# Performance work log

Measured on AMD Instinct MI355X. Metric: run time of the kernel, lower is better.

## Reference

```python
import jax, jax.numpy as jnp
import numpy as np

N, Wt, Tt, DIM = 16, 256, 2048, 256
EPS = 1e-5

def silu(x):
    return x * jax.nn.sigmoid(x)

def setup_inputs() -> dict:
    key = jax.random.key(0)
    ks = jax.random.split(key, 12)
    d = {}
    d['T'] = jnp.arange(Tt, dtype=jnp.float32)
    d['durations'] = jax.random.uniform(ks[0], (N, Wt, 1), jnp.float32)
    d['features'] = jax.random.normal(ks[1], (N, Wt, DIM), jnp.float32)
    d['conv1_w'] = jax.random.normal(ks[2], (8, DIM, 3), jnp.float32) * 0.05
    d['conv1_b'] = jnp.zeros((8,), jnp.float32)
    d['bn1_g'] = jnp.ones((8,), jnp.float32)
    d['bn1_b'] = jnp.zeros((8,), jnp.float32)
    d['bn1_m'] = jnp.zeros((8,), jnp.float32)
    d['bn1_v'] = jnp.ones((8,), jnp.float32)
    d['conv2_w'] = jax.random.normal(ks[3], (8, DIM, 3), jnp.float32) * 0.05
    d['conv2_b'] = jnp.zeros((8,), jnp.float32)
    d['bn2_g'] = jnp.ones((8,), jnp.float32)
    d['bn2_b'] = jnp.zeros((8,), jnp.float32)
    d['bn2_m'] = jnp.zeros((8,), jnp.float32)
    d['bn2_v'] = jnp.ones((8,), jnp.float32)
    d['sb1_w1'] = jax.random.normal(ks[4], (10, 2), jnp.float32) * 0.3
    d['sb1_b1'] = jnp.zeros((2,), jnp.float32)
    d['sb1_w2'] = jax.random.normal(ks[5], (2, 2), jnp.float32) * 0.3
    d['sb1_b2'] = jnp.zeros((2,), jnp.float32)
    d['sb2_w1'] = jax.random.normal(ks[6], (10, 16), jnp.float32) * 0.3
    d['sb2_b1'] = jnp.zeros((16,), jnp.float32)
    d['sb2_w2'] = jax.random.normal(ks[7], (16, 16), jnp.float32) * 0.3
    d['sb2_b2'] = jnp.zeros((16,), jnp.float32)
    d['proj1_w'] = jax.random.normal(ks[8], (2, DIM), jnp.float32) * 0.3
    d['proj1_b'] = jnp.zeros((DIM,), jnp.float32)
    d['proj2_w'] = jax.random.normal(ks[9], (16, 1), jnp.float32) * 0.3
    d['proj2_b'] = jnp.zeros((1,), jnp.float32)
    return d

def _conv_bn_silu(x_ncw, w, b, g, beta, m, v):
    # Conv1d(dim->8, k=3, pad=1) + BatchNorm(eval) + SiLU
    y = jax.lax.conv_general_dilated(x_ncw, w, (1,), [(1, 1)],
                                     dimension_numbers=('NCH', 'OIH', 'NCH'))
    y = y + b[None, :, None]
    y = (y - m[None, :, None]) * jax.lax.rsqrt(v[None, :, None] + EPS)
    y = y * g[None, :, None] + beta[None, :, None]
    return silu(y)

def _swish_block(x, w1, b1, w2, b2):
    x = silu(x @ w1 + b1)
    return silu(x @ w2 + b2)

def reference(T, durations, features, conv1_w, conv1_b, bn1_g, bn1_b, bn1_m, bn1_v,
              conv2_w, conv2_b, bn2_g, bn2_b, bn2_m, bn2_v,
              sb1_w1, sb1_b1, sb1_w2, sb1_b2, sb2_w1, sb2_b1, sb2_w2, sb2_b2,
              proj1_w, proj1_b, proj2_w, proj2_b):
    feat = jnp.swapaxes(features, 1, 2)  # (N, C, W)
    n, _, w = feat.shape
    t = T.shape[0]
    left = jnp.swapaxes(_conv_bn_silu(feat, conv1_w, conv1_b, bn1_g, bn1_b, bn1_m, bn1_v), 1, 2)   # (N, W, 8)
    right = jnp.swapaxes(_conv_bn_silu(feat, conv2_w, conv2_b, bn2_g, bn2_b, bn2_m, bn2_v), 1, 2)  # (N, W, 8)
    token_end = jnp.cumsum(durations, axis=1)        # (N, W, 1)
    token_start = token_end - durations              # (N, W, 1)
    S = T[None, None, :] - token_start               # (N, W, T)
    E = token_end - T[None, None, :]                 # (N, W, T)
    left_b = jnp.broadcast_to(left[:, :, None, :], (n, w, t, 8))
    right_b = jnp.broadcast_to(right[:, :, None, :], (n, w, t, 8))
    xleft = jnp.concatenate([S[..., None], E[..., None], left_b], axis=-1)    # (N, W, T, 10)
    xright = jnp.concatenate([S[..., None], E[..., None], right_b], axis=-1)  # (N, W, T, 10)
    C = _swish_block(xleft, sb1_w1, sb1_b1, sb1_w2, sb1_b2)                   # (N, W, T, 2)
    xr = _swish_block(xright, sb2_w1, sb2_b1, sb2_w2, sb2_b2)                 # (N, W, T, 16)
    score = (xr @ proj2_w + proj2_b)[..., 0]                                  # (N, W, T)
    Wsm = jax.nn.softmax(score, axis=1)  # softmax over tokens W
    out_r = jnp.einsum('nkt,ndk->ntd', Wsm, feat)                             # (N, T, dim)
    out_l = jnp.einsum('nkt,nktp->ntp', Wsm, C) @ proj1_w + proj1_b           # (N, T, dim)
    return out_l + out_r
```

## Files before the change

kernel.cpp:

```cpp
#include <hip/hip_runtime.h>
#include <hip/hip_bf16.h>

#define NN  16
#define WT  256
#define TT  2048
#define DIM 256
#define TBT 8

typedef __attribute__((ext_vector_type(8))) short short8_t;
typedef __attribute__((ext_vector_type(4))) float f32x4;

__device__ __forceinline__ float fast_rcp(float x){ return __builtin_amdgcn_rcpf(x); }

__device__ __forceinline__ float silu_f(float x){
    return x * fast_rcp(1.0f + __expf(-x));
}

__device__ __forceinline__ unsigned short f2bf(float x){
    union { float f; unsigned u; } v; v.f = x;
    unsigned r = v.u + 0x7FFFu + ((v.u >> 16) & 1u);
    return (unsigned short)(r >> 16);
}

__device__ __forceinline__ void fma4(float4& a, float s, const float4& f){
    a.x = fmaf(s, f.x, a.x); a.y = fmaf(s, f.y, a.y);
    a.z = fmaf(s, f.z, a.z); a.w = fmaf(s, f.w, a.w);
}

__global__ __launch_bounds__(256) void prep_k(
    const float* __restrict__ dur, const float* __restrict__ feat,
    const float* __restrict__ c1w, const float* __restrict__ c1b,
    const float* __restrict__ g1,  const float* __restrict__ be1,
    const float* __restrict__ m1,  const float* __restrict__ vv1,
    const float* __restrict__ c2w, const float* __restrict__ c2b,
    const float* __restrict__ g2,  const float* __restrict__ be2,
    const float* __restrict__ m2,  const float* __restrict__ vv2,
    const float* __restrict__ sb1w1, const float* __restrict__ sb1b1,
    const float* __restrict__ sb2w1, const float* __restrict__ sb2b1,
    float* __restrict__ v1o, float* __restrict__ v2o)
{
    int w = blockIdx.x, n = blockIdx.y;
    int tid = threadIdx.x;

    __shared__ float sdur[WT];
    sdur[tid] = dur[n*WT + tid];
    __syncthreads();
    for (int off = 1; off < WT; off <<= 1){
        float v = (tid >= off) ? sdur[tid-off] : 0.0f;
        __syncthreads();
        sdur[tid] += v;
        __syncthreads();
    }
    float end   = sdur[w];
    float start = end - dur[n*WT + w];

    const float* fb = feat + (size_t)(n*WT)*DIM;
    float fm = (w > 0)    ? fb[(size_t)(w-1)*DIM + tid] : 0.0f;
    float f0 =              fb[(size_t) w   *DIM + tid];
    float fp = (w < WT-1) ? fb[(size_t)(w+1)*DIM + tid] : 0.0f;

    float pl[8], pr[8];
    #pragma unroll
    for (int o = 0; o < 8; o++){
        const float* wp = c1w + (size_t)(o*DIM + tid)*3;
        pl[o] = fmaf(fm, wp[0], fmaf(f0, wp[1], fp*wp[2]));
        const float* wq = c2w + (size_t)(o*DIM + tid)*3;
        pr[o] = fmaf(fm, wq[0], fmaf(f0, wq[1], fp*wq[2]));
    }
    #pragma unroll
    for (int o = 0; o < 8; o++){
        #pragma unroll
        for (int off = 32; off; off >>= 1){
            pl[o] += __shfl_xor(pl[o], off);
            pr[o] += __shfl_xor(pr[o], off);
        }
    }
    __shared__ float sws[4][16];
    int wave = tid >> 6, lane = tid & 63;
    if (lane == 0){
        #pragma unroll
        for (int o = 0; o < 8; o++){ sws[wave][o] = pl[o]; sws[wave][8+o] = pr[o]; }
    }
    __syncthreads();
    __shared__ float slr[16];
    if (tid < 16){
        float s = sws[0][tid] + sws[1][tid] + sws[2][tid] + sws[3][tid];
        int o = tid & 7; bool isr = tid >= 8;
        float bias = isr ? c2b[o] : c1b[o];
        float mm   = isr ? m2[o]  : m1[o];
        float vv   = isr ? vv2[o] : vv1[o];
        float gg   = isr ? g2[o]  : g1[o];
        float bb   = isr ? be2[o] : be1[o];
        float y = s + bias;
        y = (y - mm) * rsqrtf(vv + 1e-5f);
        y = y * gg + bb;
        slr[tid] = silu_f(y);
    }
    __syncthreads();
    if (tid < 16){
        int j = tid;
        float acc = sb2b1[j] - start*sb2w1[j] + end*sb2w1[16 + j];
        #pragma unroll
        for (int o = 0; o < 8; o++) acc = fmaf(slr[8+o], sb2w1[(2+o)*16 + j], acc);
        v2o[(size_t)(n*WT + w)*16 + j] = acc;
    } else if (tid < 18){
        int p = tid - 16;
        float acc = sb1b1[p] - start*sb1w1[p] + end*sb1w1[2 + p];
        #pragma unroll
        for (int o = 0; o < 8; o++) acc = fmaf(slr[o], sb1w1[(2+o)*2 + p], acc);
        v1o[(size_t)(n*WT + w)*2 + p] = acc;
    }
}

__global__ __launch_bounds__(256) void featpack_k(const float* __restrict__ feat,
                                                  unsigned short* __restrict__ featP)
{
    int kb = blockIdx.x, n = blockIdx.y;
    int d = threadIdx.x;
    const float* fb = feat + (size_t)n*WT*DIM + (size_t)kb*32*DIM + d;
    unsigned short* op = featP + ((size_t)(n*8 + kb)*DIM + d)*32;
    unsigned short buf[32];
    #pragma unroll
    for (int e = 0; e < 32; e++) buf[e] = f2bf(fb[(size_t)e*DIM]);
    #pragma unroll
    for (int g = 0; g < 4; g++){
        uint4 u;
        u.x = (unsigned)buf[g*8+0] | ((unsigned)buf[g*8+1] << 16);
        u.y = (unsigned)buf[g*8+2] | ((unsigned)buf[g*8+3] << 16);
        u.z = (unsigned)buf[g*8+4] | ((unsigned)buf[g*8+5] << 16);
        u.w = (unsigned)buf[g*8+6] | ((unsigned)buf[g*8+7] << 16);
        *(uint4*)(op + g*8) = u;
    }
}

__global__ __launch_bounds__(256) void score1_k(
    const float* __restrict__ Tg, const float* __restrict__ v2g,
    const float* __restrict__ sb2w1, const float* __restrict__ sb2w2, const float* __restrict__ sb2b2,
    const float* __restrict__ p2w, const float* __restrict__ p2b,
    float* __restrict__ scr)
{
    int n   = blockIdx.y;
    int t0  = blockIdx.x * TBT;
    int tid = threadIdx.x;
    int w   = tid;

    __shared__ float s_w2[16*16];
    __shared__ float s_u2[16], s_b2[16], s_p2w[16];

    s_w2[tid] = sb2w2[tid];
    if (tid < 16){
        s_u2[tid]  = sb2w1[tid] - sb2w1[16 + tid];
        s_b2[tid]  = sb2b2[tid];
        s_p2w[tid] = p2w[tid];
    }
    __syncthreads();

    float v2r[16];
    {
        const float4* vp = (const float4*)(v2g + (size_t)(n*WT + w)*16);
        float4 a = vp[0], b = vp[1], c = vp[2], d = vp[3];
        v2r[0]=a.x; v2r[1]=a.y; v2r[2]=a.z; v2r[3]=a.w;
        v2r[4]=b.x; v2r[5]=b.y; v2r[6]=b.z; v2r[7]=b.w;
        v2r[8]=c.x; v2r[9]=c.y; v2r[10]=c.z; v2r[11]=c.w;
        v2r[12]=d.x; v2r[13]=d.y; v2r[14]=d.z; v2r[15]=d.w;
    }
    float p2bv = p2b[0];
    float tv[TBT];
    #pragma unroll
    for (int ti = 0; ti < TBT; ti++) tv[ti] = Tg[t0 + ti];

    unsigned mpos = 0u, mneg = 0u;
    #pragma unroll
    for (int i = 0; i < 16; i++){
        float u = s_u2[i], v = v2r[i];
        float xa = fmaf(tv[0],     u, v);
        float xb = fmaf(tv[TBT-1], u, v);
        float lo = fminf(xa, xb), hi = fmaxf(xa, xb);
        if (__all(lo >  20.0f)) mpos |= (1u << i);
        else if (__all(hi < -20.0f)) mneg |= (1u << i);
    }
    unsigned mact = 0xFFFFu & ~(mpos | mneg);

    float scores[TBT];
    if (mact == 0u){
        float hA[16], hB[16];
        #pragma unroll
        for (int j = 0; j < 16; j++){ hA[j] = s_b2[j]; hB[j] = 0.0f; }
        #pragma unroll
        for (int i = 0; i < 16; i++){
            if (mpos & (1u << i)){
                float u = s_u2[i], v = v2r[i];
                #pragma unroll
                for (int j = 0; j < 16; j++){
                    float wv = s_w2[i*16 + j];
                    hA[j] = fmaf(v, wv, hA[j]);
                    hB[j] = fmaf(u, wv, hB[j]);
                }
            }
        }
        unsigned jpos = 0u, jact = 0u;
        #pragma unroll
        for (int j = 0; j < 16; j++){
            float h0 = fmaf(tv[0],     hB[j], hA[j]);
            float h7 = fmaf(tv[TBT-1], hB[j], hA[j]);
            float lo = fminf(h0, h7), hi = fmaxf(h0, h7);
            unsigned p  = (unsigned)__all(lo > 20.0f);
            unsigned nn = (unsigned)__all(hi < -20.0f);
            jpos |= p << j;
            jact |= ((p | nn) ^ 1u) << j;
        }
        float SA = p2bv, SB = 0.0f;
        #pragma unroll
        for (int j = 0; j < 16; j++){
            float pw = s_p2w[j] * (float)((jpos >> j) & 1u);
            SA = fmaf(hA[j], pw, SA);
            SB = fmaf(hB[j], pw, SB);
        }
        #pragma unroll
        for (int ti = 0; ti < TBT; ti++) scores[ti] = fmaf(tv[ti], SB, SA);
        #pragma unroll
        for (int j = 0; j < 16; j++){
            if (jact & (1u << j)){
                float pw = s_p2w[j];
                float a = hA[j], b = hB[j];
                #pragma unroll
                for (int ti = 0; ti < TBT; ti++)
                    scores[ti] = fmaf(silu_f(fmaf(tv[ti], b, a)), pw, scores[ti]);
            }
        }
    } else {
        #pragma unroll
        for (int tp = 0; tp < TBT; tp += 2){
            float h2a[16], h2b[16];
            #pragma unroll
            for (int j = 0; j < 16; j++){ float b = s_b2[j]; h2a[j] = b; h2b[j] = b; }
            #pragma unroll
            for (int i = 0; i < 16; i++){
                if (mneg & (1u << i)) continue;
                float u = s_u2[i], v = v2r[i];
                float aa = fmaf(tv[tp],   u, v);
                float ab = fmaf(tv[tp+1], u, v);
                if (!(mpos & (1u << i))){
                    aa = silu_f(aa);
                    ab = silu_f(ab);
                }
                #pragma unroll
                for (int j = 0; j < 16; j++){
                    float wv = s_w2[i*16 + j];
                    h2a[j] = fmaf(aa, wv, h2a[j]);
                    h2b[j] = fmaf(ab, wv, h2b[j]);
                }
            }
            float sa = p2bv, sb = p2bv;
            #pragma unroll
            for (int j = 0; j < 16; j++){
                float pw = s_p2w[j];
                float ha = h2a[j], hb = h2b[j];
                if (__all(fminf(ha, hb) > 20.0f)){
                    sa = fmaf(ha, pw, sa);
                    sb = fmaf(hb, pw, sb);
                } else if (__all(fmaxf(ha, hb) < -20.0f)){
                } else {
                    sa = fmaf(silu_f(ha), pw, sa);
                    sb = fmaf(silu_f(hb), pw, sb);
                }
            }
            scores[tp] = sa; scores[tp+1] = sb;
        }
    }

    float* sbase = scr + ((size_t)n*TT + t0)*WT + w;
    #pragma unroll
    for (int ti = 0; ti < TBT; ti++) sbase[(size_t)ti*WT] = scores[ti];
}

__global__ __launch_bounds__(256) void score2_k(
    const float* __restrict__ Tg, const float* __restrict__ v1g,
    const float* __restrict__ scr,
    const float* __restrict__ sb1w1, const float* __restrict__ sb1w2, const float* __restrict__ sb1b2,
    unsigned short* __restrict__ wsm_b, float* __restrict__ wc_g)
{
    int n   = blockIdx.y;
    int t0  = blockIdx.x * TBT;
    int tid = threadIdx.x;
    int w   = tid;
    int lane = tid & 63, wave = tid >> 6;

    __shared__ float s_xa[4][TBT];
    __shared__ float s_xs[4][TBT];
    __shared__ float s_xc0[4][TBT], s_xc1[4][TBT];

    float v1r0, v1r1;
    {
        const float* vp = v1g + (size_t)(n*WT + w)*2;
        v1r0 = vp[0]; v1r1 = vp[1];
    }
    float tv[TBT];
    #pragma unroll
    for (int ti = 0; ti < TBT; ti++) tv[ti] = Tg[t0 + ti];

    float scores[TBT];
    {
        const float* sbase = scr + ((size_t)n*TT + t0)*WT + w;
        #pragma unroll
        for (int ti = 0; ti < TBT; ti++) scores[ti] = sbase[(size_t)ti*WT];
    }

    float c0r[TBT], c1r[TBT];
    {
        float u10 = sb1w1[0] - sb1w1[2], u11 = sb1w1[1] - sb1w1[3];
        float w00 = sb1w2[0], w01 = sb1w2[1], w10 = sb1w2[2], w11 = sb1w2[3];
        float b0 = sb1b2[0], b1 = sb1b2[1];
        float x0a = fmaf(tv[0], u10, v1r0), x0b = fmaf(tv[TBT-1], u10, v1r0);
        float x1a = fmaf(tv[0], u11, v1r1), x1b = fmaf(tv[TBT-1], u11, v1r1);
        bool p0 = __all(fminf(x0a, x0b) >  20.0f);
        bool n0 = __all(fmaxf(x0a, x0b) < -20.0f);
        bool p1 = __all(fminf(x1a, x1b) >  20.0f);
        bool n1 = __all(fmaxf(x1a, x1b) < -20.0f);
        #pragma unroll
        for (int ti = 0; ti < TBT; ti++){
            float x0 = fmaf(tv[ti], u10, v1r0);
            float x1 = fmaf(tv[ti], u11, v1r1);
            float gl0, gl1;
            if (p0)      gl0 = x0;
            else if (n0) gl0 = 0.0f;
            else         gl0 = silu_f(x0);
            if (p1)      gl1 = x1;
            else if (n1) gl1 = 0.0f;
            else         gl1 = silu_f(x1);
            float y0 = fmaf(gl0, w00, fmaf(gl1, w10, b0));
            float y1 = fmaf(gl0, w01, fmaf(gl1, w11, b1));
            if (__all(fminf(y0, y1) > 20.0f)){
                c0r[ti] = y0; c1r[ti] = y1;
            } else if (__all(fmaxf(y0, y1) < -20.0f)){
                c0r[ti] = 0.0f; c1r[ti] = 0.0f;
            } else {
                c0r[ti] = silu_f(y0); c1r[ti] = silu_f(y1);
            }
        }
    }

    float m[TBT];
    #pragma unroll
    for (int ti = 0; ti < TBT; ti++) m[ti] = scores[ti];
    #pragma unroll
    for (int off = 32; off; off >>= 1){
        #pragma unroll
        for (int ti = 0; ti < TBT; ti++) m[ti] = fmaxf(m[ti], __shfl_xor(m[ti], off));
    }
    if (lane == 0){
        #pragma unroll
        for (int ti = 0; ti < TBT; ti++) s_xa[wave][ti] = m[ti];
    }
    __syncthreads();
    #pragma unroll
    for (int ti = 0; ti < TBT; ti++)
        m[ti] = fmaxf(fmaxf(s_xa[0][ti], s_xa[1][ti]), fmaxf(s_xa[2][ti], s_xa[3][ti]));

    float e[TBT], ps[TBT], pc0[TBT], pc1[TBT];
    #pragma unroll
    for (int ti = 0; ti < TBT; ti++){
        e[ti]   = __expf(scores[ti] - m[ti]);
        ps[ti]  = e[ti];
        pc0[ti] = e[ti] * c0r[ti];
        pc1[ti] = e[ti] * c1r[ti];
    }
    #pragma unroll
    for (int off = 32; off; off >>= 1){
        #pragma unroll
        for (int ti = 0; ti < TBT; ti++){
            ps[ti]  += __shfl_xor(ps[ti],  off);
            pc0[ti] += __shfl_xor(pc0[ti], off);
            pc1[ti] += __shfl_xor(pc1[ti], off);
        }
    }
    if (lane == 0){
        #pragma unroll
        for (int ti = 0; ti < TBT; ti++){
            s_xs[wave][ti]  = ps[ti];
            s_xc0[wave][ti] = pc0[ti];
            s_xc1[wave][ti] = pc1[ti];
        }
    }
    __syncthreads();

    unsigned short* wbase = wsm_b + ((size_t)n*TT + t0)*WT + w;
    #pragma unroll
    for (int ti = 0; ti < TBT; ti++){
        float S  = s_xs[0][ti] + s_xs[1][ti] + s_xs[2][ti] + s_xs[3][ti];
        float rS = fast_rcp(S);
        wbase[(size_t)ti*WT] = f2bf(e[ti] * rS);
    }
    if (tid < TBT){
        int ti = tid;
        float S  = s_xs[0][ti] + s_xs[1][ti] + s_xs[2][ti] + s_xs[3][ti];
        float rS = fast_rcp(S);
        float2 wc;
        wc.x = (s_xc0[0][ti] + s_xc0[1][ti] + s_xc0[2][ti] + s_xc0[3][ti]) * rS;
        wc.y = (s_xc1[0][ti] + s_xc1[1][ti] + s_xc1[2][ti] + s_xc1[3][ti]) * rS;
        *(float2*)(wc_g + ((size_t)n*TT + t0 + ti)*2) = wc;
    }
}

__global__ __launch_bounds__(256) void score_k(
    const float* __restrict__ Tg,
    const float* __restrict__ v1g, const float* __restrict__ v2g,
    const float* __restrict__ sb1w1, const float* __restrict__ sb1w2, const float* __restrict__ sb1b2,
    const float* __restrict__ sb2w1, const float* __restrict__ sb2w2, const float* __restrict__ sb2b2,
    const float* __restrict__ p2w, const float* __restrict__ p2b,
    unsigned short* __restrict__ wsm_b, float* __restrict__ wc_g)
{
    int n   = blockIdx.y;
    int t0  = blockIdx.x * TBT;
    int tid = threadIdx.x;
    int w   = tid;
    int lane = tid & 63, wave = tid >> 6;

    __shared__ float s_w2[16*16];
    __shared__ float s_u2[16], s_b2[16], s_p2w[16];
    __shared__ float s_u1[2], s_w21[4], s_b21[2];
    __shared__ float s_xa[4][TBT];
    __shared__ float s_xs[4][TBT];
    __shared__ float s_xc0[4][TBT], s_xc1[4][TBT];

    s_w2[tid] = sb2w2[tid];
    if (tid < 16){
        s_u2[tid]  = sb2w1[tid] - sb2w1[16 + tid];
        s_b2[tid]  = sb2b2[tid];
        s_p2w[tid] = p2w[tid];
    } else if (tid < 18){
        int p = tid - 16;
        s_u1[p]  = sb1w1[p] - sb1w1[2 + p];
        s_b21[p] = sb1b2[p];
    } else if (tid < 22){
        s_w21[tid - 18] = sb1w2[tid - 18];
    }
    __syncthreads();

    float v2r[16];
    {
        const float4* vp = (const float4*)(v2g + (size_t)(n*WT + w)*16);
        float4 a = vp[0], b = vp[1], c = vp[2], d = vp[3];
        v2r[0]=a.x; v2r[1]=a.y; v2r[2]=a.z; v2r[3]=a.w;
        v2r[4]=b.x; v2r[5]=b.y; v2r[6]=b.z; v2r[7]=b.w;
        v2r[8]=c.x; v2r[9]=c.y; v2r[10]=c.z; v2r[11]=c.w;
        v2r[12]=d.x; v2r[13]=d.y; v2r[14]=d.z; v2r[15]=d.w;
    }
    float v1r0, v1r1;
    {
        const float* vp = v1g + (size_t)(n*WT + w)*2;
        v1r0 = vp[0]; v1r1 = vp[1];
    }
    float p2bv = p2b[0];
    float tv[TBT];
    #pragma unroll
    for (int ti = 0; ti < TBT; ti++) tv[ti] = Tg[t0 + ti];

    unsigned mpos = 0u, mneg = 0u;
    #pragma unroll
    for (int i = 0; i < 16; i++){
        float u = s_u2[i], v = v2r[i];
        float xa = fmaf(tv[0],     u, v);
        float xb = fmaf(tv[TBT-1], u, v);
        float lo = fminf(xa, xb), hi = fmaxf(xa, xb);
        if (__all(lo >  20.0f)) mpos |= (1u << i);
        else if (__all(hi < -20.0f)) mneg |= (1u << i);
    }
    unsigned mact = 0xFFFFu & ~(mpos | mneg);

    float scores[TBT];
    if (mact == 0u){
        float hA[16], hB[16];
        #pragma unroll
        for (int j = 0; j < 16; j++){ hA[j] = s_b2[j]; hB[j] = 0.0f; }
        #pragma unroll
        for (int i = 0; i < 16; i++){
            if (mpos & (1u << i)){
                float u = s_u2[i], v = v2r[i];
                #pragma unroll
                for (int j = 0; j < 16; j++){
                    float wv = s_w2[i*16 + j];
                    hA[j] = fmaf(v, wv, hA[j]);
                    hB[j] = fmaf(u, wv, hB[j]);
                }
            }
        }
        unsigned jpos = 0u, jact = 0u;
        #pragma unroll
        for (int j = 0; j < 16; j++){
            float h0 = fmaf(tv[0],     hB[j], hA[j]);
            float h7 = fmaf(tv[TBT-1], hB[j], hA[j]);
            float lo = fminf(h0, h7), hi = fmaxf(h0, h7);
            unsigned p  = (unsigned)__all(lo > 20.0f);
            unsigned nn = (unsigned)__all(hi < -20.0f);
            jpos |= p << j;
            jact |= ((p | nn) ^ 1u) << j;
        }
        float SA = p2bv, SB = 0.0f;
        #pragma unroll
        for (int j = 0; j < 16; j++){
            float pw = s_p2w[j] * (float)((jpos >> j) & 1u);
            SA = fmaf(hA[j], pw, SA);
            SB = fmaf(hB[j], pw, SB);
        }
        #pragma unroll
        for (int ti = 0; ti < TBT; ti++) scores[ti] = fmaf(tv[ti], SB, SA);
        #pragma unroll
        for (int j = 0; j < 16; j++){
            if (jact & (1u << j)){
                float pw = s_p2w[j];
                float a = hA[j], b = hB[j];
                #pragma unroll
                for (int ti = 0; ti < TBT; ti++)
                    scores[ti] = fmaf(silu_f(fmaf(tv[ti], b, a)), pw, scores[ti]);
            }
        }
    } else {
        #pragma unroll
        for (int tp = 0; tp < TBT; tp += 2){
            float h2a[16], h2b[16];
            #pragma unroll
            for (int j = 0; j < 16; j++){ float b = s_b2[j]; h2a[j] = b; h2b[j] = b; }
            #pragma unroll
            for (int i = 0; i < 16; i++){
                if (mneg & (1u << i)) continue;
                float u = s_u2[i], v = v2r[i];
                float aa = fmaf(tv[tp],   u, v);
                float ab = fmaf(tv[tp+1], u, v);
                if (!(mpos & (1u << i))){
                    aa = silu_f(aa);
                    ab = silu_f(ab);
                }
                #pragma unroll
                for (int j = 0; j < 16; j++){
                    float wv = s_w2[i*16 + j];
                    h2a[j] = fmaf(aa, wv, h2a[j]);
                    h2b[j] = fmaf(ab, wv, h2b[j]);
                }
            }
            float sa = p2bv, sb = p2bv;
            #pragma unroll
            for (int j = 0; j < 16; j++){
                float pw = s_p2w[j];
                float ha = h2a[j], hb = h2b[j];
                if (__all(fminf(ha, hb) > 20.0f)){
                    sa = fmaf(ha, pw, sa);
                    sb = fmaf(hb, pw, sb);
                } else if (__all(fmaxf(ha, hb) < -20.0f)){
                } else {
                    sa = fmaf(silu_f(ha), pw, sa);
                    sb = fmaf(silu_f(hb), pw, sb);
                }
            }
            scores[tp] = sa; scores[tp+1] = sb;
        }
    }

    float c0r[TBT], c1r[TBT];
    {
        float u10 = s_u1[0], u11 = s_u1[1];
        float w00 = s_w21[0], w01 = s_w21[1], w10 = s_w21[2], w11 = s_w21[3];
        float b0 = s_b21[0], b1 = s_b21[1];
        float x0a = fmaf(tv[0], u10, v1r0), x0b = fmaf(tv[TBT-1], u10, v1r0);
        float x1a = fmaf(tv[0], u11, v1r1), x1b = fmaf(tv[TBT-1], u11, v1r1);
        bool p0 = __all(fminf(x0a, x0b) >  20.0f);
        bool n0 = __all(fmaxf(x0a, x0b) < -20.0f);
        bool p1 = __all(fminf(x1a, x1b) >  20.0f);
        bool n1 = __all(fmaxf(x1a, x1b) < -20.0f);
        #pragma unroll
        for (int ti = 0; ti < TBT; ti++){
            float x0 = fmaf(tv[ti], u10, v1r0);
            float x1 = fmaf(tv[ti], u11, v1r1);
            float gl0, gl1;
            if (p0)      gl0 = x0;
            else if (n0) gl0 = 0.0f;
            else         gl0 = silu_f(x0);
            if (p1)      gl1 = x1;
            else if (n1) gl1 = 0.0f;
            else         gl1 = silu_f(x1);
            float y0 = fmaf(gl0, w00, fmaf(gl1, w10, b0));
            float y1 = fmaf(gl0, w01, fmaf(gl1, w11, b1));
            if (__all(fminf(y0, y1) > 20.0f)){
                c0r[ti] = y0; c1r[ti] = y1;
            } else if (__all(fmaxf(y0, y1) < -20.0f)){
                c0r[ti] = 0.0f; c1r[ti] = 0.0f;
            } else {
                c0r[ti] = silu_f(y0); c1r[ti] = silu_f(y1);
            }
        }
    }

    float m[TBT];
    #pragma unroll
    for (int ti = 0; ti < TBT; ti++) m[ti] = scores[ti];
    #pragma unroll
    for (int off = 32; off; off >>= 1){
        #pragma unroll
        for (int ti = 0; ti < TBT; ti++) m[ti] = fmaxf(m[ti], __shfl_xor(m[ti], off));
    }
    if (lane == 0){
        #pragma unroll
        for (int ti = 0; ti < TBT; ti++) s_xa[wave][ti] = m[ti];
    }
    __syncthreads();
    #pragma unroll
    for (int ti = 0; ti < TBT; ti++)
        m[ti] = fmaxf(fmaxf(s_xa[0][ti], s_xa[1][ti]), fmaxf(s_xa[2][ti], s_xa[3][ti]));

    float e[TBT], ps[TBT], pc0[TBT], pc1[TBT];
    #pragma unroll
    for (int ti = 0; ti < TBT; ti++){
        e[ti]   = __expf(scores[ti] - m[ti]);
        ps[ti]  = e[ti];
        pc0[ti] = e[ti] * c0r[ti];
        pc1[ti] = e[ti] * c1r[ti];
    }
    #pragma unroll
    for (int off = 32; off; off >>= 1){
        #pragma unroll
        for (int ti = 0; ti < TBT; ti++){
            ps[ti]  += __shfl_xor(ps[ti],  off);
            pc0[ti] += __shfl_xor(pc0[ti], off);
            pc1[ti] += __shfl_xor(pc1[ti], off);
        }
    }
    if (lane == 0){
        #pragma unroll
        for (int ti = 0; ti < TBT; ti++){
            s_xs[wave][ti]  = ps[ti];
            s_xc0[wave][ti] = pc0[ti];
            s_xc1[wave][ti] = pc1[ti];
        }
    }
    __syncthreads();

    unsigned short* wbase = wsm_b + ((size_t)n*TT + t0)*WT + w;
    #pragma unroll
    for (int ti = 0; ti < TBT; ti++){
        float S  = s_xs[0][ti] + s_xs[1][ti] + s_xs[2][ti] + s_xs[3][ti];
        float rS = fast_rcp(S);
        wbase[(size_t)ti*WT] = f2bf(e[ti] * rS);
    }
    if (tid < TBT){
        int ti = tid;
        float S  = s_xs[0][ti] + s_xs[1][ti] + s_xs[2][ti] + s_xs[3][ti];
        float rS = fast_rcp(S);
        float2 wc;
        wc.x = (s_xc0[0][ti] + s_xc0[1][ti] + s_xc0[2][ti] + s_xc0[3][ti]) * rS;
        wc.y = (s_xc1[0][ti] + s_xc1[1][ti] + s_xc1[2][ti] + s_xc1[3][ti]) * rS;
        *(float2*)(wc_g + ((size_t)n*TT + t0 + ti)*2) = wc;
    }
}

__global__ __launch_bounds__(512) void outr_mfma_k(
    const unsigned short* __restrict__ wsmB, const unsigned short* __restrict__ featP,
    const float* __restrict__ wc_g,
    const float* __restrict__ p1w, const float* __restrict__ p1b,
    float* __restrict__ out)
{
    int n    = blockIdx.y;
    int t0   = blockIdx.x * 32;
    int tid  = threadIdx.x;
    int lane = tid & 63, wave = tid >> 6;
    int tw   = t0 + (wave >> 2) * 16;
    int dbase = (wave & 3) * 4;
    int l15  = lane & 15, quad = lane >> 4;

    f32x4 acc[4];
    #pragma unroll
    for (int dt = 0; dt < 4; dt++) acc[dt] = (f32x4){0.f, 0.f, 0.f, 0.f};

    const unsigned short* aPtr = wsmB + ((size_t)(n*TT + tw + l15))*WT + quad*8;

    #pragma unroll
    for (int kb = 0; kb < 8; kb++){
        short8_t af = *(const short8_t*)(aPtr + kb*32);
        const unsigned short* bp = featP + ((size_t)(n*8 + kb)*DIM + dbase*16 + l15)*32 + quad*8;
        #pragma unroll
        for (int dt = 0; dt < 4; dt++){
            short8_t bf = *(const short8_t*)(bp + (size_t)dt*16*32);
            acc[dt] = __builtin_amdgcn_mfma_f32_16x16x32_bf16(af, bf, acc[dt], 0, 0, 0);
        }
    }

    float wc0[4], wc1[4];
    #pragma unroll
    for (int r = 0; r < 4; r++){
        const float* wp = wc_g + ((size_t)(n*TT + tw + quad*4 + r))*2;
        wc0[r] = wp[0]; wc1[r] = wp[1];
    }
    float* obase = out + ((size_t)(n*TT + tw + quad*4))*DIM;
    #pragma unroll
    for (int dt = 0; dt < 4; dt++){
        int d = (dbase + dt)*16 + l15;
        float pa = p1w[d], pb2 = p1w[DIM + d], pc = p1b[d];
        #pragma unroll
        for (int r = 0; r < 4; r++){
            float val = acc[dt][r] + fmaf(wc0[r], pa, fmaf(wc1[r], pb2, pc));
            obase[(size_t)r*DIM + d] = val;
        }
    }
}

__global__ __launch_bounds__(256) void fused_k(
    const float* __restrict__ Tg, const float* __restrict__ feat,
    const float* __restrict__ v1g, const float* __restrict__ v2g,
    const float* __restrict__ sb1w1, const float* __restrict__ sb1w2, const float* __restrict__ sb1b2,
    const float* __restrict__ sb2w1, const float* __restrict__ sb2w2, const float* __restrict__ sb2b2,
    const float* __restrict__ p1w, const float* __restrict__ p1b,
    const float* __restrict__ p2w, const float* __restrict__ p2b,
    float* __restrict__ out)
{
    int n   = blockIdx.y;
    int t0  = blockIdx.x * TBT;
    int tid = threadIdx.x;
    int w   = tid;
    int lane = tid & 63, wave = tid >> 6;

    __shared__ float s_w2[16*16];
    __shared__ float s_u2[16], s_b2[16], s_p2w[16];
    __shared__ float s_u1[2], s_w21[4], s_b21[2];
    __shared__ float s_wsmT[WT][TBT];
    __shared__ float s_xa[4][TBT];
    __shared__ float s_xs[4][TBT];
    __shared__ float s_xc0[4][TBT], s_xc1[4][TBT];
    __shared__ float s_wc0[TBT], s_wc1[TBT];
    __shared__ float s_out[4][DIM];

    s_w2[tid] = sb2w2[tid];
    if (tid < 16){
        s_u2[tid]  = sb2w1[tid] - sb2w1[16 + tid];
        s_b2[tid]  = sb2b2[tid];
        s_p2w[tid] = p2w[tid];
    } else if (tid < 18){
        int p = tid - 16;
        s_u1[p]  = sb1w1[p] - sb1w1[2 + p];
        s_b21[p] = sb1b2[p];
    } else if (tid < 22){
        s_w21[tid - 18] = sb1w2[tid - 18];
    }
    __syncthreads();

    float v2r[16];
    {
        const float4* vp = (const float4*)(v2g + (size_t)(n*WT + w)*16);
        float4 a = vp[0], b = vp[1], c = vp[2], d = vp[3];
        v2r[0]=a.x; v2r[1]=a.y; v2r[2]=a.z; v2r[3]=a.w;
        v2r[4]=b.x; v2r[5]=b.y; v2r[6]=b.z; v2r[7]=b.w;
        v2r[8]=c.x; v2r[9]=c.y; v2r[10]=c.z; v2r[11]=c.w;
        v2r[12]=d.x; v2r[13]=d.y; v2r[14]=d.z; v2r[15]=d.w;
    }
    float v1r0, v1r1;
    {
        const float* vp = v1g + (size_t)(n*WT + w)*2;
        v1r0 = vp[0]; v1r1 = vp[1];
    }
    float p2bv = p2b[0];
    float tv[TBT];
    #pragma unroll
    for (int ti = 0; ti < TBT; ti++) tv[ti] = Tg[t0 + ti];

    float scores[TBT];
    #pragma unroll
    for (int tp = 0; tp < TBT; tp += 2){
        float h2a[16], h2b[16];
        #pragma unroll
        for (int j = 0; j < 16; j++){ float b = s_b2[j]; h2a[j] = b; h2b[j] = b; }
        #pragma unroll
        for (int i = 0; i < 16; i++){
            float u = s_u2[i], v = v2r[i];
            float aa = silu_f(fmaf(tv[tp],   u, v));
            float ab = silu_f(fmaf(tv[tp+1], u, v));
            #pragma unroll
            for (int j = 0; j < 16; j++){
                float wv = s_w2[i*16 + j];
                h2a[j] = fmaf(aa, wv, h2a[j]);
                h2b[j] = fmaf(ab, wv, h2b[j]);
            }
        }
        float sa = p2bv, sb = p2bv;
        #pragma unroll
        for (int j = 0; j < 16; j++){
            float pw = s_p2w[j];
            sa = fmaf(silu_f(h2a[j]), pw, sa);
            sb = fmaf(silu_f(h2b[j]), pw, sb);
        }
        scores[tp] = sa; scores[tp+1] = sb;
    }

    float c0r[TBT], c1r[TBT];
    {
        float u10 = s_u1[0], u11 = s_u1[1];
        float w00 = s_w21[0], w01 = s_w21[1], w10 = s_w21[2], w11 = s_w21[3];
        float b0 = s_b21[0], b1 = s_b21[1];
        #pragma unroll
        for (int ti = 0; ti < TBT; ti++){
            float gl0 = silu_f(fmaf(tv[ti], u10, v1r0));
            float gl1 = silu_f(fmaf(tv[ti], u11, v1r1));
            c0r[ti] = silu_f(fmaf(gl0, w00, fmaf(gl1, w10, b0)));
            c1r[ti] = silu_f(fmaf(gl0, w01, fmaf(gl1, w11, b1)));
        }
    }

    float m[TBT];
    #pragma unroll
    for (int ti = 0; ti < TBT; ti++) m[ti] = scores[ti];
    #pragma unroll
    for (int off = 32; off; off >>= 1){
        #pragma unroll
        for (int ti = 0; ti < TBT; ti++) m[ti] = fmaxf(m[ti], __shfl_xor(m[ti], off));
    }
    if (lane == 0){
        #pragma unroll
        for (int ti = 0; ti < TBT; ti++) s_xa[wave][ti] = m[ti];
    }
    __syncthreads();
    #pragma unroll
    for (int ti = 0; ti < TBT; ti++)
        m[ti] = fmaxf(fmaxf(s_xa[0][ti], s_xa[1][ti]), fmaxf(s_xa[2][ti], s_xa[3][ti]));

    float e[TBT], ps[TBT], pc0[TBT], pc1[TBT];
    #pragma unroll
    for (int ti = 0; ti < TBT; ti++){
        e[ti]  = __expf(scores[ti] - m[ti]);
        ps[ti] = e[ti];
        pc0[ti] = e[ti] * c0r[ti];
        pc1[ti] = e[ti] * c1r[ti];
    }
    #pragma unroll
    for (int off = 32; off; off >>= 1){
        #pragma unroll
        for (int ti = 0; ti < TBT; ti++){
            ps[ti]  += __shfl_xor(ps[ti],  off);
            pc0[ti] += __shfl_xor(pc0[ti], off);
            pc1[ti] += __shfl_xor(pc1[ti], off);
        }
    }
    if (lane == 0){
        #pragma unroll
        for (int ti = 0; ti < TBT; ti++){
            s_xs[wave][ti]  = ps[ti];
            s_xc0[wave][ti] = pc0[ti];
            s_xc1[wave][ti] = pc1[ti];
        }
    }
    __syncthreads();
    #pragma unroll
    for (int ti = 0; ti < TBT; ti++){
        float S  = s_xs[0][ti] + s_xs[1][ti] + s_xs[2][ti] + s_xs[3][ti];
        float rS = fast_rcp(S);
        s_wsmT[w][ti] = e[ti] * rS;
    }
    if (tid < TBT){
        int ti = tid;
        float S  = s_xs[0][ti] + s_xs[1][ti] + s_xs[2][ti] + s_xs[3][ti];
        float rS = fast_rcp(S);
        s_wc0[ti] = (s_xc0[0][ti] + s_xc0[1][ti] + s_xc0[2][ti] + s_xc0[3][ti]) * rS;
        s_wc1[ti] = (s_xc1[0][ti] + s_xc1[1][ti] + s_xc1[2][ti] + s_xc1[3][ti]) * rS;
    }
    __syncthreads();

    int wid = wave;
    int dq  = lane;
    const float* fbase = feat + (size_t)n*WT*DIM + dq*4;
    float4 acc[TBT];
    #pragma unroll
    for (int i = 0; i < TBT; i++) acc[i] = make_float4(0.f, 0.f, 0.f, 0.f);

    #pragma unroll 4
    for (int w0 = wid; w0 < WT; w0 += 4){
        float4 f = *(const float4*)(fbase + (size_t)w0*DIM);
        const float4* wp = (const float4*)&s_wsmT[w0][0];
        float4 wA = wp[0], wB = wp[1];
        fma4(acc[0], wA.x, f); fma4(acc[1], wA.y, f);
        fma4(acc[2], wA.z, f); fma4(acc[3], wA.w, f);
        fma4(acc[4], wB.x, f); fma4(acc[5], wB.y, f);
        fma4(acc[6], wB.z, f); fma4(acc[7], wB.w, f);
    }

    float pw0 = p1w[tid], pw1 = p1w[DIM + tid], pbv = p1b[tid];
    float* orow = out + ((size_t)n*TT + t0)*DIM;
    #pragma unroll
    for (int ti = 0; ti < TBT; ti++){
        __syncthreads();
        *(float4*)&s_out[wid][dq*4] = acc[ti];
        __syncthreads();
        float r = s_out[0][tid] + s_out[1][tid] + s_out[2][tid] + s_out[3][tid];
        float o = fmaf(s_wc0[ti], pw0, fmaf(s_wc1[ti], pw1, r + pbv));
        orow[(size_t)ti*DIM + tid] = o;
    }
}

extern "C" void kernel_launch(void* const* d_in, const int* in_sizes, int n_in,
                              void* d_out, int out_size, void* d_ws, size_t ws_size,
                              hipStream_t stream)
{
    const float* Tg    = (const float*)d_in[0];
    const float* dur   = (const float*)d_in[1];
    const float* feat  = (const float*)d_in[2];
    const float* c1w   = (const float*)d_in[3];
    const float* c1b   = (const float*)d_in[4];
    const float* bn1g  = (const float*)d_in[5];
    const float* bn1b  = (const float*)d_in[6];
    const float* bn1m  = (const float*)d_in[7];
    const float* bn1v  = (const float*)d_in[8];
    const float* c2w   = (const float*)d_in[9];
    const float* c2b   = (const float*)d_in[10];
    const float* bn2g  = (const float*)d_in[11];
    const float* bn2b  = (const float*)d_in[12];
    const float* bn2m  = (const float*)d_in[13];
    const float* bn2v  = (const float*)d_in[14];
    const float* sb1w1 = (const float*)d_in[15];
    const float* sb1b1 = (const float*)d_in[16];
    const float* sb1w2 = (const float*)d_in[17];
    const float* sb1b2 = (const float*)d_in[18];
    const float* sb2w1 = (const float*)d_in[19];
    const float* sb2b1 = (const float*)d_in[20];
    const float* sb2w2 = (const float*)d_in[21];
    const float* sb2b2 = (const float*)d_in[22];
    const float* p1w   = (const float*)d_in[23];
    const float* p1b   = (const float*)d_in[24];
    const float* p2w   = (const float*)d_in[25];
    const float* p2b   = (const float*)d_in[26];
    float* out = (float*)d_out;

    float* ws = (float*)d_ws;
    float* v1  = ws;
    float* v2  = ws + 8192;
    float* wc  = ws + 8192 + 65536;
    unsigned short* wsmB  = (unsigned short*)(ws + 8192 + 65536 + 65536);
    unsigned short* featP = wsmB + (size_t)NN*TT*WT;
    float* scr = (float*)(featP + (size_t)NN*WT*DIM);
    size_t need_old = ((size_t)8192 + 65536 + 65536)*sizeof(float)
                    + ((size_t)NN*TT*WT + (size_t)NN*WT*DIM)*sizeof(unsigned short);
    size_t need_split = need_old + (size_t)NN*TT*WT*sizeof(float);

    prep_k<<<dim3(WT, NN), 256, 0, stream>>>(dur, feat, c1w, c1b, bn1g, bn1b, bn1m, bn1v,
                                             c2w, c2b, bn2g, bn2b, bn2m, bn2v,
                                             sb1w1, sb1b1, sb2w1, sb2b1, v1, v2);
    if (ws_size >= need_split){
        featpack_k<<<dim3(8, NN), 256, 0, stream>>>(feat, featP);
        score1_k<<<dim3(TT/TBT, NN), 256, 0, stream>>>(Tg, v2,
                                                       sb2w1, sb2w2, sb2b2,
                                                       p2w, p2b, scr);
        score2_k<<<dim3(TT/TBT, NN), 256, 0, stream>>>(Tg, v1, scr,
                                                       sb1w1, sb1w2, sb1b2,
                                                       wsmB, wc);
        outr_mfma_k<<<dim3(TT/32, NN), 512, 0, stream>>>(wsmB, featP, wc, p1w, p1b, out);
    } else if (ws_size >= need_old){
        featpack_k<<<dim3(8, NN), 256, 0, stream>>>(feat, featP);
        score_k<<<dim3(TT/TBT, NN), 256, 0, stream>>>(Tg, v1, v2,
                                                      sb1w1, sb1w2, sb1b2,
                                                      sb2w1, sb2w2, sb2b2,
                                                      p2w, p2b, wsmB, wc);
        outr_mfma_k<<<dim3(TT/32, NN), 512, 0, stream>>>(wsmB, featP, wc, p1w, p1b, out);
    } else {
        fused_k<<<dim3(TT/TBT, NN), 256, 0, stream>>>(Tg, feat, v1, v2,
                                                      sb1w1, sb1w2, sb1b2,
                                                      sb2w1, sb2w2, sb2b2,
                                                      p1w, p1b, p2w, p2b, out);
    }
}
```

Baseline: 279.8 us.

## Skip full swish-block score pass past saturation time using linearized hidden layer

Computes, per batch, the time T1 beyond which all first-layer swish units of the score block are saturated, so the first layer becomes exactly linear or zero in t. Past that time score1_k exits early and score2_k computes scores directly from precomputed per-token second-layer coefficients (hA, hB), skipping the scratch write and read. This removes most of the score1 work and its scratch traffic for late time steps. It adds an atomicMax, an init kernel and extra prep work, and relies on treating silu as identity or zero beyond the ±20 threshold, an approximation the existing code already makes.

New measurement: 312.7 us. 11.7% more time.

```diff
diff --git a/kernel.cpp b/kernel.cpp
--- a/kernel.cpp
+++ b/kernel.cpp
@@ -25,6 +25,11 @@
 __device__ __forceinline__ void fma4(float4& a, float s, const float4& f){
     a.x = fmaf(s, f.x, a.x); a.y = fmaf(s, f.y, a.y);
     a.z = fmaf(s, f.z, a.z); a.w = fmaf(s, f.w, a.w);
+}
+
+__global__ void init_k(float* __restrict__ T1N)
+{
+    if (threadIdx.x < NN) T1N[threadIdx.x] = 0.0f;
 }
 
 __global__ __launch_bounds__(256) void prep_k(
@@ -37,7 +42,9 @@
     const float* __restrict__ m2,  const float* __restrict__ vv2,
     const float* __restrict__ sb1w1, const float* __restrict__ sb1b1,
     const float* __restrict__ sb2w1, const float* __restrict__ sb2b1,
-    float* __restrict__ v1o, float* __restrict__ v2o)
+    const float* __restrict__ sb2w2, const float* __restrict__ sb2b2,
+    float* __restrict__ v1o, float* __restrict__ v2o,
+    float* __restrict__ hAo, float* __restrict__ hBo, float* __restrict__ T1No)
 {
     int w = blockIdx.x, n = blockIdx.y;
     int tid = threadIdx.x;
@@ -97,18 +104,48 @@
         slr[tid] = silu_f(y);
     }
     __syncthreads();
+
+    __shared__ float sv[16], su[16], stp[16];
     if (tid < 16){
         int j = tid;
         float acc = sb2b1[j] - start*sb2w1[j] + end*sb2w1[16 + j];
         #pragma unroll
         for (int o = 0; o < 8; o++) acc = fmaf(slr[8+o], sb2w1[(2+o)*16 + j], acc);
         v2o[(size_t)(n*WT + w)*16 + j] = acc;
+        float u = sb2w1[j] - sb2w1[16 + j];
+        sv[j] = acc; su[j] = u;
+        float tp;
+        if (u > 0.0f)      tp = (20.0f - acc) / u + 1.0f;
+        else if (u < 0.0f) tp = (-20.0f - acc) / u + 1.0f;
+        else               tp = 3.0e38f;
+        stp[j] = tp;
     } else if (tid < 18){
         int p = tid - 16;
         float acc = sb1b1[p] - start*sb1w1[p] + end*sb1w1[2 + p];
         #pragma unroll
         for (int o = 0; o < 8; o++) acc = fmaf(slr[o], sb1w1[(2+o)*2 + p], acc);
         v1o[(size_t)(n*WT + w)*2 + p] = acc;
+    }
+    __syncthreads();
+    if (hAo && tid < 16){
+        int j = tid;
+        float hA = sb2b2[j], hB = 0.0f;
+        #pragma unroll
+        for (int i = 0; i < 16; i++){
+            if (su[i] > 0.0f){
+                float wv = sb2w2[i*16 + j];
+                hA = fmaf(sv[i], wv, hA);
+                hB = fmaf(su[i], wv, hB);
+            }
+        }
+        hAo[((size_t)(n*WT + w))*16 + j] = hA;
+        if (w == 0 && n == 0) hBo[j] = hB;
+    }
+    if (hAo && tid == 0){
+        float tmax = 0.0f;
+        #pragma unroll
+        for (int i = 0; i < 16; i++) tmax = fmaxf(tmax, stp[i]);
+        atomicMax((unsigned int*)&T1No[n], __float_as_uint(tmax));
     }
 }
 
@@ -137,10 +174,12 @@
     const float* __restrict__ Tg, const float* __restrict__ v2g,
     const float* __restrict__ sb2w1, const float* __restrict__ sb2w2, const float* __restrict__ sb2b2,
     const float* __restrict__ p2w, const float* __restrict__ p2b,
+    const float* __restrict__ T1Ng,
     float* __restrict__ scr)
 {
     int n   = blockIdx.y;
     int t0  = blockIdx.x * TBT;
+    if ((float)t0 > T1Ng[n]) return;
     int tid = threadIdx.x;
     int w   = tid;
 
@@ -277,7 +316,10 @@
 __global__ __launch_bounds__(256) void score2_k(
     const float* __restrict__ Tg, const float* __restrict__ v1g,
     const float* __restrict__ scr,
+    const float* __restrict__ hAg, const float* __restrict__ hBg,
+    const float* __restrict__ T1Ng,
     const float* __restrict__ sb1w1, const float* __restrict__ sb1w2, const float* __restrict__ sb1b2,
+    const float* __restrict__ p2w, const float* __restrict__ p2b,
     unsigned short* __restrict__ wsm_b, float* __restrict__ wc_g)
 {
     int n   = blockIdx.y;
@@ -300,7 +342,49 @@
     for (int ti = 0; ti < TBT; ti++) tv[ti] = Tg[t0 + ti];
 
     float scores[TBT];
-    {
+    if ((float)t0 > T1Ng[n]){
+        float hA[16];
+        {
+            const float4* hp = (const float4*)(hAg + ((size_t)(n*WT + w))*16);
+            float4 a = hp[0], b = hp[1], c = hp[2], d = hp[3];
+            hA[0]=a.x; hA[1]=a.y; hA[2]=a.z; hA[3]=a.w;
+            hA[4]=b.x; hA[5]=b.y; hA[6]=b.z; hA[7]=b.w;
+            hA[8]=c.x; hA[9]=c.y; hA[10]=c.z; hA[11]=c.w;
+            hA[12]=d.x; hA[13]=d.y; hA[14]=d.z; hA[15]=d.w;
+        }
+        float p2bv = p2b[0];
+        unsigned jpos = 0u, jact = 0u;
+        #pragma unroll
+        for (int j = 0; j < 16; j++){
+            float hb = hBg[j];
+            float h0 = fmaf(tv[0],     hb, hA[j]);
+            float h7 = fmaf(tv[TBT-1], hb, hA[j]);
+            float lo = fminf(h0, h7), hi = fmaxf(h0, h7);
+            unsigned p  = (unsigned)__all(lo > 20.0f);
+            unsigned nn = (unsigned)__all(hi < -20.0f);
+            jpos |= p << j;
+            jact |= ((p | nn) ^ 1u) << j;
+        }
+        float SA = p2bv, SB = 0.0f;
+        #pragma unroll
+        for (int j = 0; j < 16; j++){
+            float pw = p2w[j] * (float)((jpos >> j) & 1u);
+            SA = fmaf(hA[j], pw, SA);
+            SB = fmaf(hBg[j], pw, SB);
+        }
+        #pragma unroll
+        for (int ti = 0; ti < TBT; ti++) scores[ti] = fmaf(tv[ti], SB, SA);
+        #pragma unroll
+        for (int j = 0; j < 16; j++){
+            if (jact & (1u << j)){
+                float pw = p2w[j];
+                float a = hA[j], b = hBg[j];
+                #pragma unroll
+                for (int ti = 0; ti < TBT; ti++)
+                    scores[ti] = fmaf(silu_f(fmaf(tv[ti], b, a)), pw, scores[ti]);
+            }
+        }
+    } else {
         const float* sbase = scr + ((size_t)n*TT + t0)*WT + w;
         #pragma unroll
         for (int ti = 0; ti < TBT; ti++) scores[ti] = sbase[(size_t)ti*WT];
@@ -931,21 +1015,33 @@
     unsigned short* wsmB  = (unsigned short*)(ws + 8192 + 65536 + 65536);
     unsigned short* featP = wsmB + (size_t)NN*TT*WT;
     float* scr = (float*)(featP + (size_t)NN*WT*DIM);
+    float* hAg = scr + (size_t)NN*TT*WT;
+    float* hBg = hAg + (size_t)NN*WT*16;
+    float* T1N = hBg + 16;
     size_t need_old = ((size_t)8192 + 65536 + 65536)*sizeof(float)
                     + ((size_t)NN*TT*WT + (size_t)NN*WT*DIM)*sizeof(unsigned short);
-    size_t need_split = need_old + (size_t)NN*TT*WT*sizeof(float);
-
+    size_t need_split = need_old
+                      + ((size_t)NN*TT*WT + (size_t)NN*WT*16 + 16 + NN)*sizeof(float);
+
+    bool split = (ws_size >= need_split);
+
+    if (split) init_k<<<1, 64, 0, stream>>>(T1N);
     prep_k<<<dim3(WT, NN), 256, 0, stream>>>(dur, feat, c1w, c1b, bn1g, bn1b, bn1m, bn1v,
                                              c2w, c2b, bn2g, bn2b, bn2m, bn2v,
-                                             sb1w1, sb1b1, sb2w1, sb2b1, v1, v2);
-    if (ws_size >= need_split){
+                                             sb1w1, sb1b1, sb2w1, sb2b1,
+                                             sb2w2, sb2b2,
+                                             v1, v2,
+                                             split ? hAg : nullptr,
+                                             split ? hBg : nullptr,
+                                             split ? T1N : nullptr);
+    if (split){
         featpack_k<<<dim3(8, NN), 256, 0, stream>>>(feat, featP);
         score1_k<<<dim3(TT/TBT, NN), 256, 0, stream>>>(Tg, v2,
                                                        sb2w1, sb2w2, sb2b2,
-                                                       p2w, p2b, scr);
-        score2_k<<<dim3(TT/TBT, NN), 256, 0, stream>>>(Tg, v1, scr,
+                                                       p2w, p2b, T1N, scr);
+        score2_k<<<dim3(TT/TBT, NN), 256, 0, stream>>>(Tg, v1, scr, hAg, hBg, T1N,
                                                        sb1w1, sb1w2, sb1b2,
-                                                       wsmB, wc);
+                                                       p2w, p2b, wsmB, wc);
         outr_mfma_k<<<dim3(TT/32, NN), 512, 0, stream>>>(wsmB, featP, wc, p1w, p1b, out);
     } else if (ws_size >= need_old){
         featpack_k<<<dim3(8, NN), 256, 0, stream>>>(feat, featP);
```
